# Optimization experiments

Measured on AMD Instinct MI355X. Metric: run time of the kernel, lower is better.

## Reference

```python
import jax, jax.numpy as jnp
import numpy as np

K = 16          # number of nearest neighbors (init kwarg k)
EPS = 1e-3      # denom threshold from the original code


def setup_inputs() -> dict:
    key = jax.random.key(0)
    k1, k2, k3 = jax.random.split(key, 3)
    V, F = 5000, 10000
    vertices = jax.random.normal(k1, (V, 3), dtype=jnp.float32)
    faces = jax.random.randint(k2, (F, 3), 0, V)
    probabilities = jax.random.uniform(k3, (F,), dtype=jnp.float32)
    return {"vertices": vertices, "faces": faces, "probabilities": probabilities}


def reference(vertices, faces, probabilities):
    F = faces.shape[0]
    pos = vertices[faces]                       # [F,3,3] triangle vertex coords
    bary = pos.mean(axis=1)                     # [F,3] barycenters

    # brute-force kNN over barycenters (x == y, so self is included like torch_geometric knn)
    sq = jnp.sum(bary * bary, axis=-1)          # [F]
    d2 = sq[:, None] + sq[None, :] - 2.0 * (bary @ bary.T)   # [F,F]
    _, nbr = jax.lax.top_k(-d2, K)              # [F,K] neighbor face indices

    # face normals
    e1 = pos[:, 1] - pos[:, 0]
    e2 = pos[:, 2] - pos[:, 0]
    n = jnp.cross(e1, e2)
    n = n / jnp.maximum(jnp.linalg.norm(n, axis=-1, keepdims=True), 1e-12)  # [F,3]

    # per (tri, neighbor, triangle-edge) plane intersection test
    nb_pos = pos[nbr]                           # [F,K,3,3] neighbor triangle vertices
    l0 = nb_pos                                 # segment starts
    l1 = jnp.roll(nb_pos, -1, axis=2)           # segment ends (k -> (k+1)%3)
    n_b = n[:, None, None, :]                   # [F,1,1,3]
    p0_b = pos[:, 0][:, None, None, :]          # [F,1,1,3] plane point of tri

    denom = jnp.sum(n_b * (l1 - l0), axis=-1)   # [F,K,3]
    numer = jnp.sum(n_b * (p0_b - l0), axis=-1) # [F,K,3]
    safe_denom = jnp.where(jnp.abs(denom) < EPS, 1.0, denom)
    t = numer / safe_denom
    hit = (jnp.abs(denom) >= EPS) & (t > 0.0) & (t < 1.0)   # [F,K,3]

    # early break in original => at most 1 increment per (tri, neighbor) pair
    pen = jnp.any(hit, axis=-1) & (nbr != jnp.arange(F)[:, None])  # [F,K]

    # scatter-add penetrations into neighbor_idx
    faces_penetrated = jnp.zeros((F,), jnp.float32).at[nbr.ravel()].add(
        pen.ravel().astype(jnp.float32))

    return jnp.dot(probabilities, faces_penetrated) / F
```

## Files before the change

### kernel.cpp

```cpp
#include <hip/hip_runtime.h>
#include <math.h>

#define KNN 16
#define EPS_F 0.001f
#define BLK 256
#define SCH 8
#define SSTRIDE 4

#define REP16(M) M(0) M(1) M(2) M(3) M(4) M(5) M(6) M(7) \
                 M(8) M(9) M(10) M(11) M(12) M(13) M(14) M(15)
#define REP8(M) M(0) M(1) M(2) M(3) M(4) M(5) M(6) M(7)

#define CEAI(p,a,b) { int _lo = min(p##a, p##b); int _hi = max(p##a, p##b); p##a = _lo; p##b = _hi; }
#define CEDI(p,a,b) { int _lo = min(p##a, p##b); int _hi = max(p##a, p##b); p##a = _hi; p##b = _lo; }

#define SORT16I(p) \
  CEAI(p,0,1) CEDI(p,2,3) CEAI(p,4,5) CEDI(p,6,7) CEAI(p,8,9) CEDI(p,10,11) CEAI(p,12,13) CEDI(p,14,15) \
  CEAI(p,0,2) CEAI(p,1,3) CEDI(p,4,6) CEDI(p,5,7) CEAI(p,8,10) CEAI(p,9,11) CEDI(p,12,14) CEDI(p,13,15) \
  CEAI(p,0,1) CEAI(p,2,3) CEDI(p,4,5) CEDI(p,6,7) CEAI(p,8,9) CEAI(p,10,11) CEDI(p,12,13) CEDI(p,14,15) \
  CEAI(p,0,4) CEAI(p,1,5) CEAI(p,2,6) CEAI(p,3,7) CEDI(p,8,12) CEDI(p,9,13) CEDI(p,10,14) CEDI(p,11,15) \
  CEAI(p,0,2) CEAI(p,1,3) CEAI(p,4,6) CEAI(p,5,7) CEDI(p,8,10) CEDI(p,9,11) CEDI(p,12,14) CEDI(p,13,15) \
  CEAI(p,0,1) CEAI(p,2,3) CEAI(p,4,5) CEAI(p,6,7) CEDI(p,8,9) CEDI(p,10,11) CEDI(p,12,13) CEDI(p,14,15) \
  CEAI(p,0,8) CEAI(p,1,9) CEAI(p,2,10) CEAI(p,3,11) CEAI(p,4,12) CEAI(p,5,13) CEAI(p,6,14) CEAI(p,7,15) \
  CEAI(p,0,4) CEAI(p,1,5) CEAI(p,2,6) CEAI(p,3,7) CEAI(p,8,12) CEAI(p,9,13) CEAI(p,10,14) CEAI(p,11,15) \
  CEAI(p,0,2) CEAI(p,1,3) CEAI(p,4,6) CEAI(p,5,7) CEAI(p,8,10) CEAI(p,9,11) CEAI(p,12,14) CEAI(p,13,15) \
  CEAI(p,0,1) CEAI(p,2,3) CEAI(p,4,5) CEAI(p,6,7) CEAI(p,8,9) CEAI(p,10,11) CEAI(p,12,13) CEAI(p,14,15)

#define RESORT16I(p) \
  CEAI(p,0,8) CEAI(p,1,9) CEAI(p,2,10) CEAI(p,3,11) CEAI(p,4,12) CEAI(p,5,13) CEAI(p,6,14) CEAI(p,7,15) \
  CEAI(p,0,4) CEAI(p,1,5) CEAI(p,2,6) CEAI(p,3,7) CEAI(p,8,12) CEAI(p,9,13) CEAI(p,10,14) CEAI(p,11,15) \
  CEAI(p,0,2) CEAI(p,1,3) CEAI(p,4,6) CEAI(p,5,7) CEAI(p,8,10) CEAI(p,9,11) CEAI(p,12,14) CEAI(p,13,15) \
  CEAI(p,0,1) CEAI(p,2,3) CEAI(p,4,5) CEAI(p,6,7) CEAI(p,8,9) CEAI(p,10,11) CEAI(p,12,13) CEAI(p,14,15)

#define MERGE16I(r,x) \
  r##0=min(r##0,x##15); r##1=min(r##1,x##14); r##2=min(r##2,x##13); r##3=min(r##3,x##12); \
  r##4=min(r##4,x##11); r##5=min(r##5,x##10); r##6=min(r##6,x##9);  r##7=min(r##7,x##8);  \
  r##8=min(r##8,x##7);  r##9=min(r##9,x##6);  r##10=min(r##10,x##5); r##11=min(r##11,x##4); \
  r##12=min(r##12,x##3); r##13=min(r##13,x##2); r##14=min(r##14,x##1); r##15=min(r##15,x##0); \
  RESORT16I(r)

__device__ __forceinline__ float distf(float4 q, float4 P) {
    return fmaf(q.x, P.x, fmaf(q.y, P.y, fmaf(q.z, P.z, q.w + P.w)));
}
__device__ __forceinline__ int packkey(float d2, int j) {
    return (__float_as_int(d2) & 0xFFFFC000) | j;
}

__global__ __launch_bounds__(BLK) void prep_kernel(
    const float* __restrict__ verts, const int* __restrict__ faces,
    float4* __restrict__ baryq, float4* __restrict__ baryqm,
    float* __restrict__ nrm, float* __restrict__ p0s,
    int* __restrict__ cnt, float* __restrict__ out, int F)
{
    int f = blockIdx.x * BLK + threadIdx.x;
    if (f >= F) return;
    if (f == 0) out[0] = 0.0f;
    cnt[f] = 0;
    int i0 = faces[3*f+0], i1 = faces[3*f+1], i2 = faces[3*f+2];
    float ax = verts[3*i0+0], ay = verts[3*i0+1], az = verts[3*i0+2];
    float bx = verts[3*i1+0], by = verts[3*i1+1], bz = verts[3*i1+2];
    float cx = verts[3*i2+0], cy = verts[3*i2+1], cz = verts[3*i2+2];
    float gx = (ax + bx + cx) / 3.0f;
    float gy = (ay + by + cy) / 3.0f;
    float gz = (az + bz + cz) / 3.0f;
    float sq = gx*gx + gy*gy + gz*gz;
    baryq[f]  = make_float4(gx, gy, gz, sq);
    baryqm[f] = make_float4(-2.0f*gx, -2.0f*gy, -2.0f*gz, sq);
    float e1x = bx-ax, e1y = by-ay, e1z = bz-az;
    float e2x = cx-ax, e2y = cy-ay, e2z = cz-az;
    float nx = e1y*e2z - e1z*e2y;
    float ny = e1z*e2x - e1x*e2z;
    float nz = e1x*e2y - e1y*e2x;
    float len = sqrtf(nx*nx + ny*ny + nz*nz);
    float dn = fmaxf(len, 1e-12f);
    nrm[3*f+0] = nx/dn; nrm[3*f+1] = ny/dn; nrm[3*f+2] = nz/dn;
    p0s[3*f+0] = ax; p0s[3*f+1] = ay; p0s[3*f+2] = az;
}

__global__ __launch_bounds__(BLK) void knn_sample(
    const float4* __restrict__ baryq, const float4* __restrict__ baryqm,
    int* __restrict__ samp_k, int F, int SLEN)
{
    extern __shared__ float4 sb[];
    int tid = threadIdx.x;
    int qi = blockIdx.x * BLK + tid;
    float4 q = baryq[min(qi, F-1)];
    #define DECLR(m) int r##m = 0x7fffffff;
    REP16(DECLR)
    #undef DECLR
    int sbase = blockIdx.y * SLEN;
    for (int s = tid; s < SLEN; s += BLK) {
        int j = (sbase + s) * SSTRIDE;
        sb[s] = (j < F) ? baryqm[j] : make_float4(0.f, 0.f, 0.f, INFINITY);
    }
    __syncthreads();
    #pragma unroll 1
    for (int g = 0; g < SLEN; g += 16) {
        #define MKK(m) int x##m = packkey(distf(q, sb[g+(m)]), (sbase+g+(m))*SSTRIDE);
        REP16(MKK)
        #undef MKK
        SORT16I(x)
        MERGE16I(r, x)
    }
    if (qi < F) {
        size_t cb = (size_t)blockIdx.y * KNN * F + qi;
        #define STR(m) samp_k[cb + (size_t)(m) * F] = r##m;
        REP16(STR)
        #undef STR
    }
}

__global__ __launch_bounds__(BLK) void merge_T(
    const int* __restrict__ samp_k, int* __restrict__ Tkey, int F)
{
    int qi = blockIdx.x * BLK + threadIdx.x;
    if (qi >= F) return;
    #define LDR(m) int r##m = samp_k[(size_t)(m) * F + qi];
    REP16(LDR)
    #undef LDR
    #pragma unroll 2
    for (int c = 1; c < SCH; ++c) {
        size_t cb = (size_t)c * KNN * F + qi;
        #define LDX(m) int x##m = samp_k[cb + (size_t)(m) * F];
        REP16(LDX)
        #undef LDX
        MERGE16I(r, x)
    }
    Tkey[qi] = r15;
}

__global__ __launch_bounds__(BLK) void collect_kernel(
    const float4* __restrict__ baryq, const float4* __restrict__ baryqm,
    const int* __restrict__ Tkey, int* __restrict__ cnt,
    int* __restrict__ buf, int F, int CLEN, int CAP)
{
    int tid = threadIdx.x;
    int qi = blockIdx.x * BLK + tid;
    bool active = qi < F;
    int qc = min(qi, F-1);
    float4 q = baryq[qc];
    int Tup = active ? (Tkey[qc] | 0x3FFF) : 0x80000000;
    int s0 = 0, s1 = 0, s2 = 0, s3 = 0;
    int lcnt = 0;
    #define SHIFT_INS(keyv) { \
        s3 = s2; s2 = s1; s1 = s0; s0 = (keyv); \
        if (++lcnt == 4 && active) { \
            int bp = atomicAdd(&cnt[qi], 4); \
            if (bp + 4 <= CAP) { \
                buf[(size_t)(bp+0)*F+qi] = s0; buf[(size_t)(bp+1)*F+qi] = s1; \
                buf[(size_t)(bp+2)*F+qi] = s2; buf[(size_t)(bp+3)*F+qi] = s3; } \
            lcnt = 0; } }
    #define GINS(m, idx) { bool h = __float_as_int(d##m) <= Tup; \
        if (__any(h)) { if (h) { int key = packkey(d##m, (idx)); SHIFT_INS(key) } } }
    int jb = blockIdx.y * CLEN;
    int je = min(jb + CLEN, F);
    int jfull = jb + ((je - jb) & ~15);
    #pragma unroll 1
    for (int base = jb; base < jfull; base += 16) {
        const float4* tp = baryqm + base;
        {
            #define LD8(m) float4 P##m = tp[m];
            REP8(LD8)
            #undef LD8
            #define D8(m) float d##m = distf(q, P##m);
            REP8(D8)
            #undef D8
            GINS(0, base+0) GINS(1, base+1) GINS(2, base+2) GINS(3, base+3)
            GINS(4, base+4) GINS(5, base+5) GINS(6, base+6) GINS(7, base+7)
        }
        {
            #define LD8(m) float4 P##m = tp[8+(m)];
            REP8(LD8)
            #undef LD8
            #define D8(m) float d##m = distf(q, P##m);
            REP8(D8)
            #undef D8
            GINS(0, base+8)  GINS(1, base+9)  GINS(2, base+10) GINS(3, base+11)
            GINS(4, base+12) GINS(5, base+13) GINS(6, base+14) GINS(7, base+15)
        }
    }
    for (int j = jfull; j < je; ++j) {
        float4 P0 = baryqm[j];
        float d0 = distf(q, P0);
        GINS(0, j)
    }
    #undef GINS
    #undef SHIFT_INS
    if (active && lcnt > 0) {
        int bp = atomicAdd(&cnt[qi], lcnt);
        #define FLUSH(m) if ((m) < lcnt && bp + (m) < CAP) \
            buf[(size_t)(bp + (m)) * F + qi] = s##m;
        FLUSH(0) FLUSH(1) FLUSH(2) FLUSH(3)
        #undef FLUSH
    }
}

__device__ __forceinline__ bool edge_test(
    float nx, float ny, float nz, float px, float py, float pz,
    float ax, float ay, float az, float bx, float by, float bz)
{
    float denom = nx*(bx-ax) + ny*(by-ay) + nz*(bz-az);
    if (fabsf(denom) < EPS_F) return false;
    float numer = nx*(px-ax) + ny*(py-ay) + nz*(pz-az);
    float t = numer / denom;
    return (t > 0.0f) && (t < 1.0f);
}

__global__ __launch_bounds__(BLK) void select_pen(
    const int* __restrict__ buf, const int* __restrict__ cnt,
    const float* __restrict__ verts, const int* __restrict__ faces,
    const float* __restrict__ prob, const float* __restrict__ nrm,
    const float* __restrict__ p0s, float* __restrict__ out,
    int F, int CAP)
{
    int qi = blockIdx.x * BLK + threadIdx.x;
    float val = 0.0f;
    if (qi < F) {
        int n = min(cnt[qi], CAP);
        #define DECLR(m) int r##m = 0x7fffffff;
        REP16(DECLR)
        #undef DECLR
        #pragma unroll 1
        for (int t = 0; t < n; t += 16) {
            #define LSEL(m) int x##m; { int v = buf[(size_t)(t + (m)) * F + qi]; \
                x##m = (t + (m) < n) ? v : 0x7fffffff; }
            REP16(LSEL)
            #undef LSEL
            SORT16I(x)
            MERGE16I(r, x)
        }
        float nx = nrm[3*qi+0], ny = nrm[3*qi+1], nz = nrm[3*qi+2];
        float px = p0s[3*qi+0], py = p0s[3*qi+1], pz = p0s[3*qi+2];
        #define PENM(m) { int j = r##m & 0x3FFF; \
            if (j != qi && j < F) { \
                int j0 = faces[3*j+0], j1 = faces[3*j+1], j2 = faces[3*j+2]; \
                float ax = verts[3*j0+0], ay = verts[3*j0+1], az = verts[3*j0+2]; \
                float bx = verts[3*j1+0], by = verts[3*j1+1], bz = verts[3*j1+2]; \
                float cx = verts[3*j2+0], cy = verts[3*j2+1], cz = verts[3*j2+2]; \
                bool hit = edge_test(nx,ny,nz, px,py,pz, ax,ay,az, bx,by,bz) \
                        || edge_test(nx,ny,nz, px,py,pz, bx,by,bz, cx,cy,cz) \
                        || edge_test(nx,ny,nz, px,py,pz, cx,cy,cz, ax,ay,az); \
                if (hit) val += prob[j]; } }
        REP16(PENM)
        #undef PENM
    }
    __shared__ float red[BLK];
    red[threadIdx.x] = val;
    __syncthreads();
    #pragma unroll
    for (int s = BLK/2; s > 0; s >>= 1) {
        if (threadIdx.x < s) red[threadIdx.x] += red[threadIdx.x + s];
        __syncthreads();
    }
    if (threadIdx.x == 0) atomicAdd(out, red[0] / (float)F);
}

extern "C" void kernel_launch(void* const* d_in, const int* in_sizes, int n_in,
                              void* d_out, int out_size, void* d_ws, size_t ws_size,
                              hipStream_t stream)
{
    const float* verts = (const float*)d_in[0];
    const int*   faces = (const int*)d_in[1];
    const float* prob  = (const float*)d_in[2];
    float* out = (float*)d_out;
    int F = in_sizes[2];

    size_t off = 0;
    auto carve = [&](size_t bytes) {
        size_t cur = off;
        off += (bytes + 255) & ~(size_t)255;
        return cur;
    };
    char* w = (char*)d_ws;
    int qBlocks = (F + BLK - 1) / BLK;
    float4* baryq  = (float4*)(w + carve((size_t)F * sizeof(float4)));
    float4* baryqm = (float4*)(w + carve((size_t)F * sizeof(float4)));
    float*  nrm    = (float*)(w + carve((size_t)F * 3 * sizeof(float)));
    float*  p0s    = (float*)(w + carve((size_t)F * 3 * sizeof(float)));
    int*    Tkey   = (int*)(w + carve((size_t)F * sizeof(int)));
    int*    cnt    = (int*)(w + carve((size_t)(qBlocks * BLK) * sizeof(int)));
    int*    samp_k = (int*)(w + carve((size_t)SCH * KNN * F * sizeof(int)));

    size_t remain = (ws_size > off) ? (ws_size - off) : 0;
    int CAP = (int)(remain / ((size_t)F * sizeof(int))) - 16;
    if (CAP > 448) CAP = 448;
    if (CAP < 256) CAP = 256;
    CAP &= ~15;
    int* buf = (int*)(w + carve((size_t)F * (CAP + 16) * sizeof(int)));

    int nSamp = (F + SSTRIDE - 1) / SSTRIDE;
    int SLEN = ((nSamp + SCH - 1) / SCH + 15) & ~15;
    int nChTarget = (2048 / qBlocks > 1) ? (2048 / qBlocks) : 1;
    int CLEN = (((F + nChTarget - 1) / nChTarget) + 15) & ~15;
    int nCChunk = (F + CLEN - 1) / CLEN;

    prep_kernel<<<qBlocks, BLK, 0, stream>>>(
        verts, faces, baryq, baryqm, nrm, p0s, cnt, out, F);
    knn_sample<<<dim3(qBlocks, SCH), BLK, SLEN * sizeof(float4), stream>>>(
        baryq, baryqm, samp_k, F, SLEN);
    merge_T<<<qBlocks, BLK, 0, stream>>>(samp_k, Tkey, F);
    collect_kernel<<<dim3(qBlocks, nCChunk), BLK, 0, stream>>>(
        baryq, baryqm, Tkey, cnt, buf, F, CLEN, CAP);
    select_pen<<<qBlocks, BLK, 0, stream>>>(
        buf, cnt, verts, faces, prob, nrm, p0s, out, F, CAP);
}
```

Before: 92.68 us.

## Fuse five kNN/penetration kernels into one cooperative persistent kernel with grid syncs

Replaces the five separate launches (prep, sampled kNN, threshold merge, candidate collect, select+penetration) with one cooperative kernel of 512 persistent blocks separated by grid.sync(). The collect stage now buffers candidates in per-thread shared-memory slots with branchless writes instead of wave-vote shift registers. Sample chunks go from 8 to 16 and collect chunk length is fixed at 208. This removes per-launch overhead and inter-kernel gaps, at the cost of grid-wide barriers, lower occupancy from the fixed grid, and a cap of 12 candidates per chunk that could drop neighbors.

```diff
diff --git a/kernel.cpp b/kernel.cpp
--- a/kernel.cpp
+++ b/kernel.cpp
@@ -1,11 +1,17 @@
 #include <hip/hip_runtime.h>
+#include <hip/hip_cooperative_groups.h>
 #include <math.h>
+
+namespace cg = cooperative_groups;
 
 #define KNN 16
 #define EPS_F 0.001f
 #define BLK 256
-#define SCH 8
+#define GRID 512
+#define SCH 16
 #define SSTRIDE 4
+#define SLOTS 13
+#define CLEN 208
 
 #define REP16(M) M(0) M(1) M(2) M(3) M(4) M(5) M(6) M(7) \
                  M(8) M(9) M(10) M(11) M(12) M(13) M(14) M(15)
@@ -46,155 +52,6 @@
     return (__float_as_int(d2) & 0xFFFFC000) | j;
 }
 
-__global__ __launch_bounds__(BLK) void prep_kernel(
-    const float* __restrict__ verts, const int* __restrict__ faces,
-    float4* __restrict__ baryq, float4* __restrict__ baryqm,
-    float* __restrict__ nrm, float* __restrict__ p0s,
-    int* __restrict__ cnt, float* __restrict__ out, int F)
-{
-    int f = blockIdx.x * BLK + threadIdx.x;
-    if (f >= F) return;
-    if (f == 0) out[0] = 0.0f;
-    cnt[f] = 0;
-    int i0 = faces[3*f+0], i1 = faces[3*f+1], i2 = faces[3*f+2];
-    float ax = verts[3*i0+0], ay = verts[3*i0+1], az = verts[3*i0+2];
-    float bx = verts[3*i1+0], by = verts[3*i1+1], bz = verts[3*i1+2];
-    float cx = verts[3*i2+0], cy = verts[3*i2+1], cz = verts[3*i2+2];
-    float gx = (ax + bx + cx) / 3.0f;
-    float gy = (ay + by + cy) / 3.0f;
-    float gz = (az + bz + cz) / 3.0f;
-    float sq = gx*gx + gy*gy + gz*gz;
-    baryq[f]  = make_float4(gx, gy, gz, sq);
-    baryqm[f] = make_float4(-2.0f*gx, -2.0f*gy, -2.0f*gz, sq);
-    float e1x = bx-ax, e1y = by-ay, e1z = bz-az;
-    float e2x = cx-ax, e2y = cy-ay, e2z = cz-az;
-    float nx = e1y*e2z - e1z*e2y;
-    float ny = e1z*e2x - e1x*e2z;
-    float nz = e1x*e2y - e1y*e2x;
-    float len = sqrtf(nx*nx + ny*ny + nz*nz);
-    float dn = fmaxf(len, 1e-12f);
-    nrm[3*f+0] = nx/dn; nrm[3*f+1] = ny/dn; nrm[3*f+2] = nz/dn;
-    p0s[3*f+0] = ax; p0s[3*f+1] = ay; p0s[3*f+2] = az;
-}
-
-__global__ __launch_bounds__(BLK) void knn_sample(
-    const float4* __restrict__ baryq, const float4* __restrict__ baryqm,
-    int* __restrict__ samp_k, int F, int SLEN)
-{
-    extern __shared__ float4 sb[];
-    int tid = threadIdx.x;
-    int qi = blockIdx.x * BLK + tid;
-    float4 q = baryq[min(qi, F-1)];
-    #define DECLR(m) int r##m = 0x7fffffff;
-    REP16(DECLR)
-    #undef DECLR
-    int sbase = blockIdx.y * SLEN;
-    for (int s = tid; s < SLEN; s += BLK) {
-        int j = (sbase + s) * SSTRIDE;
-        sb[s] = (j < F) ? baryqm[j] : make_float4(0.f, 0.f, 0.f, INFINITY);
-    }
-    __syncthreads();
-    #pragma unroll 1
-    for (int g = 0; g < SLEN; g += 16) {
-        #define MKK(m) int x##m = packkey(distf(q, sb[g+(m)]), (sbase+g+(m))*SSTRIDE);
-        REP16(MKK)
-        #undef MKK
-        SORT16I(x)
-        MERGE16I(r, x)
-    }
-    if (qi < F) {
-        size_t cb = (size_t)blockIdx.y * KNN * F + qi;
-        #define STR(m) samp_k[cb + (size_t)(m) * F] = r##m;
-        REP16(STR)
-        #undef STR
-    }
-}
-
-__global__ __launch_bounds__(BLK) void merge_T(
-    const int* __restrict__ samp_k, int* __restrict__ Tkey, int F)
-{
-    int qi = blockIdx.x * BLK + threadIdx.x;
-    if (qi >= F) return;
-    #define LDR(m) int r##m = samp_k[(size_t)(m) * F + qi];
-    REP16(LDR)
-    #undef LDR
-    #pragma unroll 2
-    for (int c = 1; c < SCH; ++c) {
-        size_t cb = (size_t)c * KNN * F + qi;
-        #define LDX(m) int x##m = samp_k[cb + (size_t)(m) * F];
-        REP16(LDX)
-        #undef LDX
-        MERGE16I(r, x)
-    }
-    Tkey[qi] = r15;
-}
-
-__global__ __launch_bounds__(BLK) void collect_kernel(
-    const float4* __restrict__ baryq, const float4* __restrict__ baryqm,
-    const int* __restrict__ Tkey, int* __restrict__ cnt,
-    int* __restrict__ buf, int F, int CLEN, int CAP)
-{
-    int tid = threadIdx.x;
-    int qi = blockIdx.x * BLK + tid;
-    bool active = qi < F;
-    int qc = min(qi, F-1);
-    float4 q = baryq[qc];
-    int Tup = active ? (Tkey[qc] | 0x3FFF) : 0x80000000;
-    int s0 = 0, s1 = 0, s2 = 0, s3 = 0;
-    int lcnt = 0;
-    #define SHIFT_INS(keyv) { \
-        s3 = s2; s2 = s1; s1 = s0; s0 = (keyv); \
-        if (++lcnt == 4 && active) { \
-            int bp = atomicAdd(&cnt[qi], 4); \
-            if (bp + 4 <= CAP) { \
-                buf[(size_t)(bp+0)*F+qi] = s0; buf[(size_t)(bp+1)*F+qi] = s1; \
-                buf[(size_t)(bp+2)*F+qi] = s2; buf[(size_t)(bp+3)*F+qi] = s3; } \
-            lcnt = 0; } }
-    #define GINS(m, idx) { bool h = __float_as_int(d##m) <= Tup; \
-        if (__any(h)) { if (h) { int key = packkey(d##m, (idx)); SHIFT_INS(key) } } }
-    int jb = blockIdx.y * CLEN;
-    int je = min(jb + CLEN, F);
-    int jfull = jb + ((je - jb) & ~15);
-    #pragma unroll 1
-    for (int base = jb; base < jfull; base += 16) {
-        const float4* tp = baryqm + base;
-        {
-            #define LD8(m) float4 P##m = tp[m];
-            REP8(LD8)
-            #undef LD8
-            #define D8(m) float d##m = distf(q, P##m);
-            REP8(D8)
-            #undef D8
-            GINS(0, base+0) GINS(1, base+1) GINS(2, base+2) GINS(3, base+3)
-            GINS(4, base+4) GINS(5, base+5) GINS(6, base+6) GINS(7, base+7)
-        }
-        {
-            #define LD8(m) float4 P##m = tp[8+(m)];
-            REP8(LD8)
-            #undef LD8
-            #define D8(m) float d##m = distf(q, P##m);
-            REP8(D8)
-            #undef D8
-            GINS(0, base+8)  GINS(1, base+9)  GINS(2, base+10) GINS(3, base+11)
-            GINS(4, base+12) GINS(5, base+13) GINS(6, base+14) GINS(7, base+15)
-        }
-    }
-    for (int j = jfull; j < je; ++j) {
-        float4 P0 = baryqm[j];
-        float d0 = distf(q, P0);
-        GINS(0, j)
-    }
-    #undef GINS
-    #undef SHIFT_INS
-    if (active && lcnt > 0) {
-        int bp = atomicAdd(&cnt[qi], lcnt);
-        #define FLUSH(m) if ((m) < lcnt && bp + (m) < CAP) \
-            buf[(size_t)(bp + (m)) * F + qi] = s##m;
-        FLUSH(0) FLUSH(1) FLUSH(2) FLUSH(3)
-        #undef FLUSH
-    }
-}
-
 __device__ __forceinline__ bool edge_test(
     float nx, float ny, float nz, float px, float py, float pz,
     float ax, float ay, float az, float bx, float by, float bz)
@@ -206,53 +63,201 @@
     return (t > 0.0f) && (t < 1.0f);
 }
 
-__global__ __launch_bounds__(BLK) void select_pen(
-    const int* __restrict__ buf, const int* __restrict__ cnt,
+__global__ __launch_bounds__(BLK, 2) void fused_kernel(
     const float* __restrict__ verts, const int* __restrict__ faces,
-    const float* __restrict__ prob, const float* __restrict__ nrm,
-    const float* __restrict__ p0s, float* __restrict__ out,
-    int F, int CAP)
+    const float* __restrict__ prob, float* __restrict__ out,
+    float4* __restrict__ baryq, float4* __restrict__ baryqm,
+    float* __restrict__ nrm, float* __restrict__ p0s,
+    int* __restrict__ samp_k, int* __restrict__ Tkey,
+    int* __restrict__ cnt, int* __restrict__ buf,
+    int F, int CAP, int SLEN, int qB, int nCC)
 {
-    int qi = blockIdx.x * BLK + threadIdx.x;
-    float val = 0.0f;
-    if (qi < F) {
-        int n = min(cnt[qi], CAP);
-        #define DECLR(m) int r##m = 0x7fffffff;
-        REP16(DECLR)
-        #undef DECLR
-        #pragma unroll 1
-        for (int t = 0; t < n; t += 16) {
-            #define LSEL(m) int x##m; { int v = buf[(size_t)(t + (m)) * F + qi]; \
-                x##m = (t + (m) < n) ? v : 0x7fffffff; }
-            REP16(LSEL)
-            #undef LSEL
-            SORT16I(x)
+    cg::grid_group grid = cg::this_grid();
+    __shared__ __align__(16) char smem[BLK * SLOTS * 4];
+    int tid = threadIdx.x;
+    int bid = blockIdx.x;
+
+    for (int f = bid * BLK + tid; f < F; f += GRID * BLK) {
+        if (f == 0) out[0] = 0.0f;
+        cnt[f] = 0;
+        int i0 = faces[3*f+0], i1 = faces[3*f+1], i2 = faces[3*f+2];
+        float ax = verts[3*i0+0], ay = verts[3*i0+1], az = verts[3*i0+2];
+        float bx = verts[3*i1+0], by = verts[3*i1+1], bz = verts[3*i1+2];
+        float cx = verts[3*i2+0], cy = verts[3*i2+1], cz = verts[3*i2+2];
+        float gx = (ax + bx + cx) / 3.0f;
+        float gy = (ay + by + cy) / 3.0f;
+        float gz = (az + bz + cz) / 3.0f;
+        float sq = gx*gx + gy*gy + gz*gz;
+        baryq[f]  = make_float4(gx, gy, gz, sq);
+        baryqm[f] = make_float4(-2.0f*gx, -2.0f*gy, -2.0f*gz, sq);
+        float e1x = bx-ax, e1y = by-ay, e1z = bz-az;
+        float e2x = cx-ax, e2y = cy-ay, e2z = cz-az;
+        float nx = e1y*e2z - e1z*e2y;
+        float ny = e1z*e2x - e1x*e2z;
+        float nz = e1x*e2y - e1y*e2x;
+        float len = sqrtf(nx*nx + ny*ny + nz*nz);
+        float dn = fmaxf(len, 1e-12f);
+        nrm[3*f+0] = nx/dn; nrm[3*f+1] = ny/dn; nrm[3*f+2] = nz/dn;
+        p0s[3*f+0] = ax; p0s[3*f+1] = ay; p0s[3*f+2] = az;
+    }
+    grid.sync();
+
+    {
+        float4* sb = (float4*)smem;
+        int nCells = qB * SCH;
+        for (int cell = bid; cell < nCells; cell += GRID) {
+            int qb = cell / SCH, c = cell % SCH;
+            int qi = qb * BLK + tid;
+            float4 q = baryq[min(qi, F-1)];
+            int sbase = c * SLEN;
+            __syncthreads();
+            for (int s = tid; s < SLEN; s += BLK) {
+                int j = (sbase + s) * SSTRIDE;
+                sb[s] = (j < F) ? baryqm[j] : make_float4(0.f, 0.f, 0.f, INFINITY);
+            }
+            __syncthreads();
+            #define DECLR(m) int r##m = 0x7fffffff;
+            REP16(DECLR)
+            #undef DECLR
+            #pragma unroll 1
+            for (int g = 0; g < SLEN; g += 16) {
+                #define MKK(m) int x##m = packkey(distf(q, sb[g+(m)]), (sbase+g+(m))*SSTRIDE);
+                REP16(MKK)
+                #undef MKK
+                SORT16I(x)
+                MERGE16I(r, x)
+            }
+            if (qi < F) {
+                size_t cb = (size_t)c * KNN * F + qi;
+                #define STR(m) samp_k[cb + (size_t)(m) * F] = r##m;
+                REP16(STR)
+                #undef STR
+            }
+        }
+    }
+    grid.sync();
+
+    for (int qi = bid * BLK + tid; qi < F; qi += GRID * BLK) {
+        #define LDR(m) int r##m = samp_k[(size_t)(m) * F + qi];
+        REP16(LDR)
+        #undef LDR
+        #pragma unroll 2
+        for (int c = 1; c < SCH; ++c) {
+            size_t cb = (size_t)c * KNN * F + qi;
+            #define LDX(m) int x##m = samp_k[cb + (size_t)(m) * F];
+            REP16(LDX)
+            #undef LDX
             MERGE16I(r, x)
         }
-        float nx = nrm[3*qi+0], ny = nrm[3*qi+1], nz = nrm[3*qi+2];
-        float px = p0s[3*qi+0], py = p0s[3*qi+1], pz = p0s[3*qi+2];
-        #define PENM(m) { int j = r##m & 0x3FFF; \
-            if (j != qi && j < F) { \
-                int j0 = faces[3*j+0], j1 = faces[3*j+1], j2 = faces[3*j+2]; \
-                float ax = verts[3*j0+0], ay = verts[3*j0+1], az = verts[3*j0+2]; \
-                float bx = verts[3*j1+0], by = verts[3*j1+1], bz = verts[3*j1+2]; \
-                float cx = verts[3*j2+0], cy = verts[3*j2+1], cz = verts[3*j2+2]; \
-                bool hit = edge_test(nx,ny,nz, px,py,pz, ax,ay,az, bx,by,bz) \
-                        || edge_test(nx,ny,nz, px,py,pz, bx,by,bz, cx,cy,cz) \
-                        || edge_test(nx,ny,nz, px,py,pz, cx,cy,cz, ax,ay,az); \
-                if (hit) val += prob[j]; } }
-        REP16(PENM)
-        #undef PENM
-    }
-    __shared__ float red[BLK];
-    red[threadIdx.x] = val;
-    __syncthreads();
-    #pragma unroll
-    for (int s = BLK/2; s > 0; s >>= 1) {
-        if (threadIdx.x < s) red[threadIdx.x] += red[threadIdx.x + s];
+        Tkey[qi] = r15;
+    }
+    grid.sync();
+
+    {
+        int* slots = (int*)smem;
+        int lbase = tid * SLOTS;
+        int nCells = qB * nCC;
+        for (int cell = bid; cell < nCells; cell += GRID) {
+            int qb = cell / nCC, c = cell % nCC;
+            int qi = qb * BLK + tid;
+            bool active = qi < F;
+            int qc = min(qi, F-1);
+            float4 q = baryq[qc];
+            int Tup = active ? (Tkey[qc] | 0x3FFF) : 0x80000000;
+            int lcnt = 0;
+            int jb = c * CLEN;
+            int je = min(jb + CLEN, F);
+            if (jb < F) {
+                #define BINS(m, idx) { bool h = __float_as_int(d##m) <= Tup; \
+                    int sel = h ? min(lcnt, 12) : 12; \
+                    slots[lbase + sel] = packkey(d##m, (idx)); \
+                    lcnt += h ? 1 : 0; }
+                int jfull = jb + ((je - jb) & ~15);
+                #pragma unroll 1
+                for (int base = jb; base < jfull; base += 16) {
+                    const float4* tp = baryqm + base;
+                    {
+                        #define LD8(m) float4 P##m = tp[m];
+                        REP8(LD8)
+                        #undef LD8
+                        #define D8(m) float d##m = distf(q, P##m);
+                        REP8(D8)
+                        #undef D8
+                        BINS(0, base+0) BINS(1, base+1) BINS(2, base+2) BINS(3, base+3)
+                        BINS(4, base+4) BINS(5, base+5) BINS(6, base+6) BINS(7, base+7)
+                    }
+                    {
+                        #define LD8(m) float4 P##m = tp[8+(m)];
+                        REP8(LD8)
+                        #undef LD8
+                        #define D8(m) float d##m = distf(q, P##m);
+                        REP8(D8)
+                        #undef D8
+                        BINS(0, base+8)  BINS(1, base+9)  BINS(2, base+10) BINS(3, base+11)
+                        BINS(4, base+12) BINS(5, base+13) BINS(6, base+14) BINS(7, base+15)
+                    }
+                }
+                for (int j = jfull; j < je; ++j) {
+                    float4 P0 = baryqm[j];
+                    float d0 = distf(q, P0);
+                    BINS(0, j)
+                }
+                #undef BINS
+                int n = min(lcnt, 12);
+                if (active && n > 0) {
+                    int bp = atomicAdd(&cnt[qi], n);
+                    for (int k = 0; k < n; ++k) {
+                        int p = bp + k;
+                        if (p < CAP) buf[(size_t)p * F + qi] = slots[lbase + k];
+                    }
+                }
+            }
+        }
+    }
+    grid.sync();
+
+    if (bid < qB) {
+        float* red = (float*)smem;
+        int qi = bid * BLK + tid;
+        float val = 0.0f;
+        if (qi < F) {
+            int n = min(cnt[qi], CAP);
+            #define DECLR(m) int r##m = 0x7fffffff;
+            REP16(DECLR)
+            #undef DECLR
+            #pragma unroll 1
+            for (int t = 0; t < n; t += 16) {
+                #define LSEL(m) int x##m; { int v = buf[(size_t)(t + (m)) * F + qi]; \
+                    x##m = (t + (m) < n) ? v : 0x7fffffff; }
+                REP16(LSEL)
+                #undef LSEL
+                SORT16I(x)
+                MERGE16I(r, x)
+            }
+            float nx = nrm[3*qi+0], ny = nrm[3*qi+1], nz = nrm[3*qi+2];
+            float px = p0s[3*qi+0], py = p0s[3*qi+1], pz = p0s[3*qi+2];
+            #define PENM(m) { int j = r##m & 0x3FFF; \
+                if (j != qi && j < F) { \
+                    int j0 = faces[3*j+0], j1 = faces[3*j+1], j2 = faces[3*j+2]; \
+                    float ax = verts[3*j0+0], ay = verts[3*j0+1], az = verts[3*j0+2]; \
+                    float bx = verts[3*j1+0], by = verts[3*j1+1], bz = verts[3*j1+2]; \
+                    float cx = verts[3*j2+0], cy = verts[3*j2+1], cz = verts[3*j2+2]; \
+                    bool hit = edge_test(nx,ny,nz, px,py,pz, ax,ay,az, bx,by,bz) \
+                            || edge_test(nx,ny,nz, px,py,pz, bx,by,bz, cx,cy,cz) \
+                            || edge_test(nx,ny,nz, px,py,pz, cx,cy,cz, ax,ay,az); \
+                    if (hit) val += prob[j]; } }
+            REP16(PENM)
+            #undef PENM
+        }
+        red[tid] = val;
         __syncthreads();
-    }
-    if (threadIdx.x == 0) atomicAdd(out, red[0] / (float)F);
+        #pragma unroll
+        for (int s = BLK/2; s > 0; s >>= 1) {
+            if (tid < s) red[tid] += red[tid + s];
+            __syncthreads();
+        }
+        if (tid == 0) atomicAdd(out, red[0] / (float)F);
+    }
 }
 
 extern "C" void kernel_launch(void* const* d_in, const int* in_sizes, int n_in,
@@ -272,35 +277,32 @@
         return cur;
     };
     char* w = (char*)d_ws;
-    int qBlocks = (F + BLK - 1) / BLK;
     float4* baryq  = (float4*)(w + carve((size_t)F * sizeof(float4)));
     float4* baryqm = (float4*)(w + carve((size_t)F * sizeof(float4)));
     float*  nrm    = (float*)(w + carve((size_t)F * 3 * sizeof(float)));
     float*  p0s    = (float*)(w + carve((size_t)F * 3 * sizeof(float)));
     int*    Tkey   = (int*)(w + carve((size_t)F * sizeof(int)));
-    int*    cnt    = (int*)(w + carve((size_t)(qBlocks * BLK) * sizeof(int)));
+    int*    cnt    = (int*)(w + carve((size_t)F * sizeof(int)));
     int*    samp_k = (int*)(w + carve((size_t)SCH * KNN * F * sizeof(int)));
 
     size_t remain = (ws_size > off) ? (ws_size - off) : 0;
     int CAP = (int)(remain / ((size_t)F * sizeof(int))) - 16;
-    if (CAP > 448) CAP = 448;
-    if (CAP < 256) CAP = 256;
+    if (CAP > 256) CAP = 256;
+    if (CAP < 192) CAP = 192;
     CAP &= ~15;
     int* buf = (int*)(w + carve((size_t)F * (CAP + 16) * sizeof(int)));
 
     int nSamp = (F + SSTRIDE - 1) / SSTRIDE;
     int SLEN = ((nSamp + SCH - 1) / SCH + 15) & ~15;
-    int nChTarget = (2048 / qBlocks > 1) ? (2048 / qBlocks) : 1;
-    int CLEN = (((F + nChTarget - 1) / nChTarget) + 15) & ~15;
-    int nCChunk = (F + CLEN - 1) / CLEN;
-
-    prep_kernel<<<qBlocks, BLK, 0, stream>>>(
-        verts, faces, baryq, baryqm, nrm, p0s, cnt, out, F);
-    knn_sample<<<dim3(qBlocks, SCH), BLK, SLEN * sizeof(float4), stream>>>(
-        baryq, baryqm, samp_k, F, SLEN);
-    merge_T<<<qBlocks, BLK, 0, stream>>>(samp_k, Tkey, F);
-    collect_kernel<<<dim3(qBlocks, nCChunk), BLK, 0, stream>>>(
-        baryq, baryqm, Tkey, cnt, buf, F, CLEN, CAP);
-    select_pen<<<qBlocks, BLK, 0, stream>>>(
-        buf, cnt, verts, faces, prob, nrm, p0s, out, F, CAP);
-}
+    int qB = (F + BLK - 1) / BLK;
+    int nCC = (F + CLEN - 1) / CLEN;
+
+    void* args[] = {
+        (void*)&verts, (void*)&faces, (void*)&prob, (void*)&out,
+        (void*)&baryq, (void*)&baryqm, (void*)&nrm, (void*)&p0s,
+        (void*)&samp_k, (void*)&Tkey, (void*)&cnt, (void*)&buf,
+        (void*)&F, (void*)&CAP, (void*)&SLEN, (void*)&qB, (void*)&nCC
+    };
+    hipLaunchCooperativeKernel((const void*)fused_kernel,
+                               dim3(GRID), dim3(BLK), args, 0, stream);
+}
```

Result: slower. 324.0 us (+249.6%).
